# Performance work log

Measured on AMD Instinct MI355X. Metric: run time of the kernel, lower is better.

## Reference

```python
import jax, jax.numpy as jnp
import numpy as np

B, S, D = 2, 2048, 1024
H, DK, DV = 16, 64, 64

def setup_inputs() -> dict:
    key = jax.random.key(0)
    ks = jax.random.split(key, 5)
    scale = 1.0 / np.sqrt(D)  # xavier-ish
    return {
        "Q": jax.random.normal(ks[0], (B, S, D), dtype=jnp.float32),
        "attn_mask": jax.random.uniform(ks[1], (B, S), dtype=jnp.float32),
        "W_Q": jax.random.normal(ks[2], (H * DK, D), dtype=jnp.float32) * scale,
        "b_Q": jnp.zeros((H * DK,), dtype=jnp.float32),
        "W_K": jax.random.normal(ks[3], (H * DK, D), dtype=jnp.float32) * scale,
        "b_K": jnp.zeros((H * DK,), dtype=jnp.float32),
        "W_V": jax.random.normal(ks[4], (H * DV, D), dtype=jnp.float32) * scale,
        "b_V": jnp.zeros((H * DV,), dtype=jnp.float32),
    }

def reference(Q, attn_mask, W_Q, b_Q, W_K, b_K, W_V, b_V):
    b, s, _ = Q.shape
    # projections -> [B, H, S, d]
    q = (Q @ W_Q.T + b_Q).reshape(b, s, H, DK).transpose(0, 2, 1, 3)
    k = (Q @ W_K.T + b_K).reshape(b, s, H, DK).transpose(0, 2, 1, 3)
    v = (Q @ W_V.T + b_V).reshape(b, s, H, DV).transpose(0, 2, 1, 3)
    # exp-based attention (NOT stable softmax), multiplicative mask
    scores = jnp.einsum('bhqd,bhkd->bhqk', q, k) / np.sqrt(DK)
    scores = jnp.exp(scores)
    # mask [B, S_key] broadcast over heads and queries -> [B, 1, 1, S]
    scores = scores * attn_mask[:, None, None, :]
    attn = scores / (jnp.sum(scores, axis=-1, keepdims=True) + 1e-8)
    context = jnp.einsum('bhqk,bhkd->bhqd', attn, v)
    # [B, H, S, DV] -> [B, S, H*DV]
    return context.transpose(0, 2, 1, 3).reshape(b, s, H * DV)
```

## Files before the change

### kernel.cpp

```cpp
#include <hip/hip_runtime.h>
#include <hip/hip_bf16.h>
#include <math.h>

#define BATCH  2
#define S_LEN  2048
#define DMODEL 1024
#define NH     16
#define DHEAD  64

typedef __attribute__((ext_vector_type(8))) short bf16x8;
typedef __attribute__((ext_vector_type(4))) float f32x4;

#define MFMA16(a,b,c) __builtin_amdgcn_mfma_f32_16x16x32_bf16((a),(b),(c),0,0,0)

#define QSCALE 0.18033688011110793f
#define EXP2F(x) __builtin_amdgcn_exp2f(x)

__device__ __forceinline__ unsigned int pkbf(float a, float b) {
    __hip_bfloat162 h = __float22bfloat162_rn(make_float2(a, b));
    union { __hip_bfloat162 h; unsigned int u; } v; v.h = h; return v.u;
}
__device__ __forceinline__ void gl2lds16(const void* g, void* l) {
    __builtin_amdgcn_global_load_lds(
        (const __attribute__((address_space(1))) void*)(g),
        (__attribute__((address_space(3))) void*)(l), 16, 0, 0);
}

__global__ __launch_bounds__(256) void cvt_all(
    const float* __restrict__ Q,  const float* __restrict__ WQ,
    const float* __restrict__ WK, const float* __restrict__ WV,
    const float* __restrict__ msk,
    unsigned short* __restrict__ Qbf, unsigned short* __restrict__ Wbf,
    unsigned short* __restrict__ mbf)
{
    int i = blockIdx.x * blockDim.x + threadIdx.x;
    const float* src;
    unsigned short* dst;
    int off;
    if (i < 1048576) {
        src = Q; dst = Qbf; off = i;
    } else if (i < 1835008) {
        int j = i - 1048576;
        int which = j >> 18;
        src = (which == 0) ? WQ : ((which == 1) ? WK : WV);
        dst = Wbf + ((size_t)which << 20);
        off = j & 262143;
    } else {
        int j = i - 1835008;
        if (j >= 1024) return;
        src = msk; dst = mbf; off = j;
    }
    float4 a = ((const float4*)src)[off];
    uint2 o;
    o.x = pkbf(a.x, a.y); o.y = pkbf(a.z, a.w);
    ((uint2*)dst)[off] = o;
}

__global__ __launch_bounds__(256) void proj_mfma(
    const unsigned short* __restrict__ Abf,
    const unsigned short* __restrict__ Wbf,
    const float* __restrict__ bQ, const float* __restrict__ bK,
    const float* __restrict__ bV, const float* __restrict__ mask,
    unsigned short* __restrict__ qw, unsigned short* __restrict__ kw,
    unsigned short* __restrict__ vt)
{
    __shared__ union {
        struct { unsigned short At[2][128*64]; unsigned short Bt[2][128*64]; } s;
        unsigned short Ct[128*132];
    } sm;

    const int tid  = threadIdx.x;
    const int lane = tid & 63;
    const int wv   = tid >> 6;
    const int wm   = (wv >> 1) * 64;
    const int wn   = (wv & 1) * 64;
    const int q15  = lane & 15;
    const int quad = lane >> 4;

    const int f  = blockIdx.x + (blockIdx.y << 3) + (blockIdx.z << 8);
    const int l  = (f & 7) * 96 + (f >> 3);
    const int z  = l >> 8;
    const int lr = l & 255;
    const int n0 = (lr & 7) * 128;
    const int m0 = (lr >> 3) * 128;

    const unsigned short* Wz = Wbf + (size_t)z * DMODEL * DMODEL;
    const float* bias = (z == 0) ? bQ : ((z == 1) ? bK : bV);

    f32x4 zero4 = {0.f, 0.f, 0.f, 0.f};
    f32x4 acc[4][4];
    #pragma unroll
    for (int i = 0; i < 4; ++i)
        #pragma unroll
        for (int j = 0; j < 4; ++j) acc[i][j] = zero4;

    #define STAGE_PROJ(BUF, K0)                                                \
        _Pragma("unroll")                                                      \
        for (int c = 0; c < 4; ++c) {                                          \
            int o   = tid * 16 + c * 4096;                                     \
            int row = o >> 7;                                                  \
            int lb  = (o & 127) ^ ((row & 7) << 4);                            \
            gl2lds16(Abf + (size_t)(m0 + row) * DMODEL + (K0) + (lb >> 1),     \
                     (char*)sm.s.At[BUF] + o);                                 \
            gl2lds16(Wz  + (size_t)(n0 + row) * DMODEL + (K0) + (lb >> 1),     \
                     (char*)sm.s.Bt[BUF] + o);                                 \
        }

    STAGE_PROJ(0, 0)
    __syncthreads();

    const int sw = (q15 & 7) << 4;

    for (int t = 0; t < 16; ++t) {
        const int buf = t & 1;
        if (t < 15) { STAGE_PROJ(buf ^ 1, (t + 1) * 64) }

        bf16x8 af[4][2], bfr[4][2];
        #pragma unroll
        for (int i = 0; i < 4; ++i) {
            const char* pa = (const char*)sm.s.At[buf] + (wm + i*16 + q15) * 128;
            const char* pb = (const char*)sm.s.Bt[buf] + (wn + i*16 + q15) * 128;
            af[i][0]  = *(const bf16x8*)(pa + (( 0 + quad*16) ^ sw));
            af[i][1]  = *(const bf16x8*)(pa + ((64 + quad*16) ^ sw));
            bfr[i][0] = *(const bf16x8*)(pb + (( 0 + quad*16) ^ sw));
            bfr[i][1] = *(const bf16x8*)(pb + ((64 + quad*16) ^ sw));
        }

        if (z < 2) {
            #pragma unroll
            for (int ks = 0; ks < 2; ++ks)
                #pragma unroll
                for (int i = 0; i < 4; ++i)
                    #pragma unroll
                    for (int j = 0; j < 4; ++j)
                        acc[i][j] = MFMA16(bfr[j][ks], af[i][ks], acc[i][j]);
        } else {
            #pragma unroll
            for (int ks = 0; ks < 2; ++ks)
                #pragma unroll
                for (int i = 0; i < 4; ++i)
                    #pragma unroll
                    for (int j = 0; j < 4; ++j)
                        acc[i][j] = MFMA16(af[i][ks], bfr[j][ks], acc[i][j]);
        }
        __syncthreads();
    }
    #undef STAGE_PROJ

    if (z < 2) {
        const float qs = (z == 0) ? QSCALE : 1.0f;
        #pragma unroll
        for (int i = 0; i < 4; ++i) {
            int ml = wm + i*16 + q15;
            #pragma unroll
            for (int j = 0; j < 4; ++j) {
                int nl = wn + j*16 + quad*4;
                float4 b4 = *(const float4*)(bias + n0 + nl);
                f32x4 v = acc[i][j];
                uint2 u;
                u.x = pkbf((v.x + b4.x)*qs, (v.y + b4.y)*qs);
                u.y = pkbf((v.z + b4.z)*qs, (v.w + b4.w)*qs);
                *(uint2*)&sm.Ct[ml*132 + nl] = u;
            }
        }
    } else {
        #pragma unroll
        for (int i = 0; i < 4; ++i) {
            int ml = wm + i*16 + quad*4;
            int sg = m0 + ml;
            int b2 = sg >> 11, s0g = sg & 2047;
            float4 mk4 = *(const float4*)(mask + (size_t)b2*S_LEN + s0g);
            #pragma unroll
            for (int j = 0; j < 4; ++j) {
                int nl = wn + j*16 + q15;
                float bv = bias[n0 + nl];
                f32x4 v = acc[i][j];
                uint2 u;
                u.x = pkbf((v.x + bv)*mk4.x, (v.y + bv)*mk4.y);
                u.y = pkbf((v.z + bv)*mk4.z, (v.w + bv)*mk4.w);
                *(uint2*)&sm.Ct[nl*132 + ml] = u;
            }
        }
    }
    __syncthreads();

    {
        int row  = tid >> 1;
        int half = (tid & 1) * 64;
        const uint4* src = (const uint4*)&sm.Ct[row*132 + half];
        unsigned short* dst;
        if (z < 2) {
            unsigned short* outp = (z == 0) ? qw : kw;
            int mg = m0 + row;  int b2 = mg >> 11, s = mg & 2047;
            int n  = n0 + half; int hh = n >> 6;
            dst = outp + (((size_t)b2*NH + hh)*S_LEN + s)*DHEAD;
        } else {
            int n  = n0 + row;  int hh = n >> 6, dv = n & 63;
            int b2 = m0 >> 11, s0 = m0 & 2047;
            dst = vt + (((size_t)b2*NH + hh)*DHEAD + dv)*S_LEN + s0 + half;
        }
        #pragma unroll
        for (int c = 0; c < 8; ++c) ((uint4*)dst)[c] = src[c];
    }
}

__global__ __launch_bounds__(256, 2) void attn_mfma(
    const unsigned short* __restrict__ qw, const unsigned short* __restrict__ kw,
    const unsigned short* __restrict__ vt, const unsigned short* __restrict__ mbf,
    float* __restrict__ out)
{
    __shared__ __align__(16) unsigned short Ks[2][64][64];
    __shared__ __align__(16) unsigned short Vs[2][64][64];

    const int tid  = threadIdx.x;
    const int lane = tid & 63;
    const int wv   = tid >> 6;
    const int q15  = lane & 15;
    const int quad = lane >> 4;

    const int orig = blockIdx.x + (blockIdx.y << 4) + (blockIdx.z << 8);
    const int lid  = (orig & 7) * 64 + (orig >> 3);
    const int q0   = (lid & 15) * 128;
    const int head = lid >> 4;
    const int h    = head & 15;
    const int b    = head >> 4;

    const size_t headoff = ((size_t)b * NH + h) * S_LEN * DHEAD;
    const unsigned short* qb = qw + headoff;
    const unsigned short* kb = kw + headoff;
    const unsigned short* vb = vt + headoff;
    const unsigned short* mb = mbf + (size_t)b * S_LEN;

    bf16x8 qf[2][2];
    #pragma unroll
    for (int qi = 0; qi < 2; ++qi) {
        const unsigned short* qr = qb + (size_t)(q0 + wv*32 + qi*16 + q15)*DHEAD;
        qf[qi][0] = *(const bf16x8*)(qr + quad*8);
        qf[qi][1] = *(const bf16x8*)(qr + 32 + quad*8);
    }

    const int srow = tid >> 3;
    const int kap  = (srow & 3) | (((srow >> 4) & 1) << 2) | (((srow >> 2) & 3) << 3);
    const int lb   = ((tid & 7) * 16) ^ ((srow & 7) << 4);
    const unsigned short* ksrc0 = kb + (size_t)kap        * DHEAD + (lb >> 1);
    const unsigned short* ksrc1 = kb + (size_t)(kap + 32) * DHEAD + (lb >> 1);
    const unsigned short* vsrc0 = vb + (size_t)srow        * S_LEN + (lb >> 1);
    const unsigned short* vsrc1 = vb + (size_t)(srow + 32) * S_LEN + (lb >> 1);
    char* kdst = (char*)&Ks[0][0][0] + tid * 16;
    char* vdst = (char*)&Vs[0][0][0] + tid * 16;
    const int sw = (q15 & 7) << 4;

    f32x4 zero4 = {0.f, 0.f, 0.f, 0.f};
    f32x4 oacc[2][4];
    f32x4 dacc[2];
    #pragma unroll
    for (int qi = 0; qi < 2; ++qi) {
        dacc[qi] = zero4;
        #pragma unroll
        for (int nj = 0; nj < 4; ++nj) oacc[qi][nj] = zero4;
    }

    bf16x8 pfA[2][2], pfB[2][2];
    bf16x8 vfA[4][2], vfB[4][2];

    #define ATTN_BODY(T, BUF, PFP, VFP, PFN, VFN, DOPV, DOPREF)                 \
    {                                                                           \
        const char* kbase = (const char*)&Ks[0][0][0] + (BUF) * 8192;           \
        const char* vbase = (const char*)&Vs[0][0][0] + (BUF) * 8192;           \
        _Pragma("unroll")                                                       \
        for (int nj = 0; nj < 4; ++nj) {                                        \
            const char* vrp = vbase + (nj*16 + q15) * 128;                      \
            VFN[nj][0] = *(const bf16x8*)(vrp + (( 0 + quad*16) ^ sw));         \
            VFN[nj][1] = *(const bf16x8*)(vrp + ((64 + quad*16) ^ sw));         \
        }                                                                       \
        if (DOPREF) {                                                           \
            const int kn = ((T) + 1) * 64;                                      \
            const int ob = ((BUF) ^ 1) * 8192;                                  \
            gl2lds16(ksrc0 + (size_t)kn * DHEAD, kdst + ob);                    \
            gl2lds16(ksrc1 + (size_t)kn * DHEAD, kdst + ob + 4096);             \
            gl2lds16(vsrc0 + kn, vdst + ob);                                    \
            gl2lds16(vsrc1 + kn, vdst + ob + 4096);                             \
        }                                                                       \
        bf16x8 mp0, mp1;                                                        \
        if (DOPV) {                                                             \
            mp0 = *(const bf16x8*)(mb + ((T)-1)*64 + quad*8);                   \
            mp1 = *(const bf16x8*)(mb + ((T)-1)*64 + 32 + quad*8);              \
        }                                                                       \
        f32x4 s[2][4];                                                          \
        __builtin_amdgcn_s_setprio(1);                                          \
        _Pragma("unroll")                                                       \
        for (int ks = 0; ks < 4; ++ks) {                                        \
            const char* krp = kbase + (ks*16 + q15) * 128;                      \
            bf16x8 kf0 = *(const bf16x8*)(krp + (( 0 + quad*16) ^ sw));         \
            bf16x8 kf1 = *(const bf16x8*)(krp + ((64 + quad*16) ^ sw));         \
            _Pragma("unroll")                                                   \
            for (int qi = 0; qi < 2; ++qi) {                                    \
                f32x4 a = MFMA16(kf0, qf[qi][0], zero4);                        \
                s[qi][ks] = MFMA16(kf1, qf[qi][1], a);                          \
            }                                                                   \
        }                                                                       \
        if (DOPV) {                                                             \
            _Pragma("unroll")                                                   \
            for (int qi = 0; qi < 2; ++qi) {                                    \
                dacc[qi] = MFMA16(PFP[qi][0], mp0, dacc[qi]);                   \
                dacc[qi] = MFMA16(PFP[qi][1], mp1, dacc[qi]);                   \
            }                                                                   \
            _Pragma("unroll")                                                   \
            for (int nj = 0; nj < 4; ++nj)                                      \
                _Pragma("unroll")                                               \
                for (int qi = 0; qi < 2; ++qi) {                                \
                    oacc[qi][nj] = MFMA16(PFP[qi][0], VFP[nj][0], oacc[qi][nj]);\
                    oacc[qi][nj] = MFMA16(PFP[qi][1], VFP[nj][1], oacc[qi][nj]);\
                }                                                               \
        }                                                                       \
        __builtin_amdgcn_s_setprio(0);                                          \
        _Pragma("unroll")                                                       \
        for (int qi = 0; qi < 2; ++qi) {                                        \
            uint4 u0, u1;                                                       \
            u0.x = pkbf(EXP2F(s[qi][0][0]), EXP2F(s[qi][0][1]));                \
            u0.y = pkbf(EXP2F(s[qi][0][2]), EXP2F(s[qi][0][3]));                \
            u0.z = pkbf(EXP2F(s[qi][1][0]), EXP2F(s[qi][1][1]));                \
            u0.w = pkbf(EXP2F(s[qi][1][2]), EXP2F(s[qi][1][3]));                \
            u1.x = pkbf(EXP2F(s[qi][2][0]), EXP2F(s[qi][2][1]));                \
            u1.y = pkbf(EXP2F(s[qi][2][2]), EXP2F(s[qi][2][3]));                \
            u1.z = pkbf(EXP2F(s[qi][3][0]), EXP2F(s[qi][3][1]));                \
            u1.w = pkbf(EXP2F(s[qi][3][2]), EXP2F(s[qi][3][3]));                \
            union { uint4 u; bf16x8 hh; } c0, c1;                               \
            c0.u = u0; c1.u = u1;                                               \
            PFN[qi][0] = c0.hh;                                                 \
            PFN[qi][1] = c1.hh;                                                 \
        }                                                                       \
        __syncthreads();                                                        \
    }

    gl2lds16(ksrc0, kdst);
    gl2lds16(ksrc1, kdst + 4096);
    gl2lds16(vsrc0, vdst);
    gl2lds16(vsrc1, vdst + 4096);
    __syncthreads();

    ATTN_BODY(0, 0, pfB, vfB, pfA, vfA, 0, 1)

    for (int t = 1; t < 31; t += 2) {
        ATTN_BODY(t,     1, pfA, vfA, pfB, vfB, 1, 1)
        ATTN_BODY(t + 1, 0, pfB, vfB, pfA, vfA, 1, 1)
    }

    ATTN_BODY(31, 1, pfA, vfA, pfB, vfB, 1, 0)
    #undef ATTN_BODY

    {
        bf16x8 mp0 = *(const bf16x8*)(mb + 31*64 + quad*8);
        bf16x8 mp1 = *(const bf16x8*)(mb + 31*64 + 32 + quad*8);
        #pragma unroll
        for (int qi = 0; qi < 2; ++qi) {
            dacc[qi] = MFMA16(pfB[qi][0], mp0, dacc[qi]);
            dacc[qi] = MFMA16(pfB[qi][1], mp1, dacc[qi]);
        }
        #pragma unroll
        for (int nj = 0; nj < 4; ++nj)
            #pragma unroll
            for (int qi = 0; qi < 2; ++qi) {
                oacc[qi][nj] = MFMA16(pfB[qi][0], vfB[nj][0], oacc[qi][nj]);
                oacc[qi][nj] = MFMA16(pfB[qi][1], vfB[nj][1], oacc[qi][nj]);
            }
    }

    #pragma unroll
    for (int qi = 0; qi < 2; ++qi)
        #pragma unroll
        for (int r = 0; r < 4; ++r) {
            float inv = 1.0f / (dacc[qi][r] + 1e-8f);
            size_t row = ((size_t)b*S_LEN + q0 + wv*32 + qi*16 + quad*4 + r)*DMODEL
                       + h*DHEAD;
            #pragma unroll
            for (int nj = 0; nj < 4; ++nj)
                out[row + nj*16 + q15] = oacc[qi][nj][r] * inv;
        }
}

extern "C" void kernel_launch(void* const* d_in, const int* in_sizes, int n_in,
                              void* d_out, int out_size, void* d_ws, size_t ws_size,
                              hipStream_t stream) {
    const float* Q    = (const float*)d_in[0];
    const float* msk  = (const float*)d_in[1];
    const float* W_Q  = (const float*)d_in[2];
    const float* b_Q  = (const float*)d_in[3];
    const float* W_K  = (const float*)d_in[4];
    const float* b_K  = (const float*)d_in[5];
    const float* W_V  = (const float*)d_in[6];
    const float* b_V  = (const float*)d_in[7];
    float* out = (float*)d_out;

    unsigned short* wsu = (unsigned short*)d_ws;
    unsigned short* Qbf = wsu;
    unsigned short* Wbf = Qbf + (size_t)4096*1024;
    unsigned short* qwb = Wbf + (size_t)3*1024*1024;
    unsigned short* kwb = qwb + (size_t)4*1024*1024;
    unsigned short* vtb = kwb + (size_t)4*1024*1024;
    unsigned short* mbf = vtb + (size_t)4*1024*1024;

    cvt_all<<<7172, 256, 0, stream>>>(Q, W_Q, W_K, W_V, msk, Qbf, Wbf, mbf);

    proj_mfma<<<dim3(8, 32, 3), 256, 0, stream>>>(
        Qbf, Wbf, b_Q, b_K, b_V, msk, qwb, kwb, vtb);

    attn_mfma<<<dim3(S_LEN/128, NH, BATCH), 256, 0, stream>>>(
        qwb, kwb, vtb, mbf, out);
}
```

Before: 166.2 us.

## Split attention key range across two wave groups per block and merge partials

```diff
diff --git a/kernel.cpp b/kernel.cpp
--- a/kernel.cpp
+++ b/kernel.cpp
@@ -204,19 +204,21 @@
     }
 }
 
-__global__ __launch_bounds__(256, 2) void attn_mfma(
+__global__ __launch_bounds__(512, 4) void attn_mfma(
     const unsigned short* __restrict__ qw, const unsigned short* __restrict__ kw,
     const unsigned short* __restrict__ vt, const unsigned short* __restrict__ mbf,
     float* __restrict__ out)
 {
-    __shared__ __align__(16) unsigned short Ks[2][64][64];
-    __shared__ __align__(16) unsigned short Vs[2][64][64];
+    __shared__ __align__(16) char smem[65536];
 
     const int tid  = threadIdx.x;
     const int lane = tid & 63;
-    const int wv   = tid >> 6;
+    const int w    = tid >> 6;
+    const int g    = w >> 2;
+    const int wv   = w & 3;
     const int q15  = lane & 15;
     const int quad = lane >> 4;
+    const int st   = tid & 255;
 
     const int orig = blockIdx.x + (blockIdx.y << 4) + (blockIdx.z << 8);
     const int lid  = (orig & 7) * 64 + (orig >> 3);
@@ -229,7 +231,7 @@
     const unsigned short* qb = qw + headoff;
     const unsigned short* kb = kw + headoff;
     const unsigned short* vb = vt + headoff;
-    const unsigned short* mb = mbf + (size_t)b * S_LEN;
+    const unsigned short* mg = mbf + (size_t)b * S_LEN + (g << 10);
 
     bf16x8 qf[2][2];
     #pragma unroll
@@ -239,15 +241,17 @@
         qf[qi][1] = *(const bf16x8*)(qr + 32 + quad*8);
     }
 
-    const int srow = tid >> 3;
+    const int srow = st >> 3;
     const int kap  = (srow & 3) | (((srow >> 4) & 1) << 2) | (((srow >> 2) & 3) << 3);
-    const int lb   = ((tid & 7) * 16) ^ ((srow & 7) << 4);
-    const unsigned short* ksrc0 = kb + (size_t)kap        * DHEAD + (lb >> 1);
-    const unsigned short* ksrc1 = kb + (size_t)(kap + 32) * DHEAD + (lb >> 1);
-    const unsigned short* vsrc0 = vb + (size_t)srow        * S_LEN + (lb >> 1);
-    const unsigned short* vsrc1 = vb + (size_t)(srow + 32) * S_LEN + (lb >> 1);
-    char* kdst = (char*)&Ks[0][0][0] + tid * 16;
-    char* vdst = (char*)&Vs[0][0][0] + tid * 16;
+    const int lb   = ((st & 7) * 16) ^ ((srow & 7) << 4);
+    const unsigned short* ksrc0 = kb + (size_t)((g << 10) + kap)       * DHEAD + (lb >> 1);
+    const unsigned short* ksrc1 = kb + (size_t)((g << 10) + kap + 32)  * DHEAD + (lb >> 1);
+    const unsigned short* vsrc0 = vb + (size_t)srow        * S_LEN + (g << 10) + (lb >> 1);
+    const unsigned short* vsrc1 = vb + (size_t)(srow + 32) * S_LEN + (g << 10) + (lb >> 1);
+    char* kreg = smem + g * 32768;
+    char* vreg = kreg + 16384;
+    char* kdst = kreg + st * 16;
+    char* vdst = vreg + st * 16;
     const int sw = (q15 & 7) << 4;
 
     f32x4 zero4 = {0.f, 0.f, 0.f, 0.f};
@@ -265,8 +269,8 @@
 
     #define ATTN_BODY(T, BUF, PFP, VFP, PFN, VFN, DOPV, DOPREF)                 \
     {                                                                           \
-        const char* kbase = (const char*)&Ks[0][0][0] + (BUF) * 8192;           \
-        const char* vbase = (const char*)&Vs[0][0][0] + (BUF) * 8192;           \
+        const char* kbase = kreg + (BUF) * 8192;                                \
+        const char* vbase = vreg + (BUF) * 8192;                                \
         _Pragma("unroll")                                                       \
         for (int nj = 0; nj < 4; ++nj) {                                        \
             const char* vrp = vbase + (nj*16 + q15) * 128;                      \
@@ -283,8 +287,8 @@
         }                                                                       \
         bf16x8 mp0, mp1;                                                        \
         if (DOPV) {                                                             \
-            mp0 = *(const bf16x8*)(mb + ((T)-1)*64 + quad*8);                   \
-            mp1 = *(const bf16x8*)(mb + ((T)-1)*64 + 32 + quad*8);              \
+            mp0 = *(const bf16x8*)(mg + ((T)-1)*64 + quad*8);                   \
+            mp1 = *(const bf16x8*)(mg + ((T)-1)*64 + 32 + quad*8);              \
         }                                                                       \
         f32x4 s[2][4];                                                          \
         __builtin_amdgcn_s_setprio(1);                                          \
@@ -341,17 +345,17 @@
 
     ATTN_BODY(0, 0, pfB, vfB, pfA, vfA, 0, 1)
 
-    for (int t = 1; t < 31; t += 2) {
+    for (int t = 1; t < 15; t += 2) {
         ATTN_BODY(t,     1, pfA, vfA, pfB, vfB, 1, 1)
         ATTN_BODY(t + 1, 0, pfB, vfB, pfA, vfA, 1, 1)
     }
 
-    ATTN_BODY(31, 1, pfA, vfA, pfB, vfB, 1, 0)
+    ATTN_BODY(15, 1, pfA, vfA, pfB, vfB, 1, 0)
     #undef ATTN_BODY
 
     {
-        bf16x8 mp0 = *(const bf16x8*)(mb + 31*64 + quad*8);
-        bf16x8 mp1 = *(const bf16x8*)(mb + 31*64 + 32 + quad*8);
+        bf16x8 mp0 = *(const bf16x8*)(mg + 15*64 + quad*8);
+        bf16x8 mp1 = *(const bf16x8*)(mg + 15*64 + 32 + quad*8);
         #pragma unroll
         for (int qi = 0; qi < 2; ++qi) {
             dacc[qi] = MFMA16(pfB[qi][0], mp0, dacc[qi]);
@@ -366,17 +370,35 @@
             }
     }
 
-    #pragma unroll
-    for (int qi = 0; qi < 2; ++qi)
-        #pragma unroll
-        for (int r = 0; r < 4; ++r) {
-            float inv = 1.0f / (dacc[qi][r] + 1e-8f);
-            size_t row = ((size_t)b*S_LEN + q0 + wv*32 + qi*16 + quad*4 + r)*DMODEL
-                       + h*DHEAD;
-            #pragma unroll
-            for (int nj = 0; nj < 4; ++nj)
-                out[row + nj*16 + q15] = oacc[qi][nj][r] * inv;
-        }
+    float* numL = (float*)smem;
+    float* denL = (float*)(smem + 128*68*4);
+    if (g == 1) {
+        #pragma unroll
+        for (int qi = 0; qi < 2; ++qi)
+            #pragma unroll
+            for (int r = 0; r < 4; ++r) {
+                int row = wv*32 + qi*16 + quad*4 + r;
+                #pragma unroll
+                for (int nj = 0; nj < 4; ++nj)
+                    numL[row*68 + nj*16 + q15] = oacc[qi][nj][r];
+                if (q15 == 0) denL[row] = dacc[qi][r];
+            }
+    }
+    __syncthreads();
+    if (g == 0) {
+        #pragma unroll
+        for (int qi = 0; qi < 2; ++qi)
+            #pragma unroll
+            for (int r = 0; r < 4; ++r) {
+                int row = wv*32 + qi*16 + quad*4 + r;
+                float inv = 1.0f / (dacc[qi][r] + denL[row] + 1e-8f);
+                size_t orow = ((size_t)b*S_LEN + q0 + row)*DMODEL + h*DHEAD;
+                #pragma unroll
+                for (int nj = 0; nj < 4; ++nj)
+                    out[orow + nj*16 + q15] =
+                        (oacc[qi][nj][r] + numL[row*68 + nj*16 + q15]) * inv;
+            }
+    }
 }
 
 extern "C" void kernel_launch(void* const* d_in, const int* in_sizes, int n_in,
@@ -405,6 +427,6 @@
     proj_mfma<<<dim3(8, 32, 3), 256, 0, stream>>>(
         Qbf, Wbf, b_Q, b_K, b_V, msk, qwb, kwb, vtb);
 
-    attn_mfma<<<dim3(S_LEN/128, NH, BATCH), 256, 0, stream>>>(
+    attn_mfma<<<dim3(S_LEN/128, NH, BATCH), 512, 0, stream>>>(
         qwb, kwb, vtb, mbf, out);
 }
```

After: 363.0 us. 118% more time.
